# Optimization experiments

Measured on AMD Instinct MI355X. Metric: run time of the kernel, lower is better.

## Reference

```python
import jax, jax.numpy as jnp
import numpy as np

D_MODEL = 1024
NUM_HEADS = 16
BATCH = 2
SEQ = 2048


def setup_inputs() -> dict:
    key = jax.random.key(0)
    ks = jax.random.split(key, 5)
    scale = 1.0 / np.sqrt(D_MODEL)
    x = jax.random.normal(ks[0], (BATCH, SEQ, D_MODEL), dtype=jnp.float32)
    Wq = jax.random.normal(ks[1], (D_MODEL, D_MODEL), dtype=jnp.float32) * scale
    Wk = jax.random.normal(ks[2], (D_MODEL, D_MODEL), dtype=jnp.float32) * scale
    Wv = jax.random.normal(ks[3], (D_MODEL, D_MODEL), dtype=jnp.float32) * scale
    Wo = jax.random.normal(ks[4], (D_MODEL, D_MODEL), dtype=jnp.float32) * scale
    return {"x": x, "Wq": Wq, "Wk": Wk, "Wv": Wv, "Wo": Wo}


def reference(x, Wq, Wk, Wv, Wo):
    b, s, d_model = x.shape
    h = NUM_HEADS
    d_head = d_model // h
    # projections (Linear with weight [out,in]: y = x @ W^T)
    def split_heads(y):
        return y.reshape(b, s, h, d_head).transpose(0, 2, 1, 3)  # b h s d
    q = split_heads(x @ Wq.T)
    k = split_heads(x @ Wk.T)
    v = split_heads(x @ Wv.T)
    # full (non-flash) attention, as in the original
    att = jnp.einsum('bhsd,bhtd->bhst', q, k) / jnp.sqrt(jnp.float32(d_head)).astype(x.dtype)
    att = jax.nn.softmax(att, axis=-1)
    out = jnp.einsum('bhst,bhtd->bhsd', att, v)
    out = out.transpose(0, 2, 1, 3).reshape(b, s, d_model)
    return out @ Wo.T
```

## Files before the change

kernel.cpp:

```cpp
#include <hip/hip_runtime.h>
#include <stdint.h>

typedef __bf16 bf16_t;
typedef __bf16 bf16x4 __attribute__((ext_vector_type(4)));
typedef __bf16 bf16x8 __attribute__((ext_vector_type(8)));
typedef float  f32x4  __attribute__((ext_vector_type(4)));
typedef float  f32x16 __attribute__((ext_vector_type(16)));

#define D_MODEL 1024
#define SEQ     2048
#define BATCH   2
#define NHEAD   16
#define DHEAD   64
#define NROWS   (BATCH*SEQ)
#define LDT     72

#define QSCALE  (0.125f * 1.4426950408889634f)

__device__ __forceinline__ void async_ld16(const bf16_t* g, bf16_t* l) {
    __builtin_amdgcn_global_load_lds(
        (const __attribute__((address_space(1))) uint32_t*)(uintptr_t)g,
        (__attribute__((address_space(3))) uint32_t*)(uintptr_t)l,
        16, 0, 0);
}

__device__ __forceinline__ bf16x8 cvt8(f32x4 lo, f32x4 hi) {
    bf16x8 o;
#pragma unroll
    for (int i = 0; i < 4; ++i) { o[i] = (bf16_t)lo[i]; o[4 + i] = (bf16_t)hi[i]; }
    return o;
}

__device__ __forceinline__ void plswap(uint32_t& a, uint32_t& b) {
    asm("v_permlane32_swap_b32 %0, %1" : "+v"(a), "+v"(b));
}

__global__ void __launch_bounds__(256)
k_cvt(const float* __restrict__ w0, const float* __restrict__ w1,
      const float* __restrict__ w2, const float* __restrict__ w3,
      const float* __restrict__ x,
      bf16_t* __restrict__ o0, bf16_t* __restrict__ o1,
      bf16_t* __restrict__ o2, bf16_t* __restrict__ o3,
      bf16_t* __restrict__ ox)
{
    const int blk = blockIdx.x;
    const float* s; bf16_t* d; int bi;
    if (blk < 2048) { s = x; d = ox; bi = blk; }
    else {
        const int t = blk - 2048, sel = t >> 9; bi = t & 511;
        s = (sel == 0) ? w0 : (sel == 1) ? w1 : (sel == 2) ? w2 : w3;
        d = (sel == 0) ? o0 : (sel == 1) ? o1 : (sel == 2) ? o2 : o3;
    }
    const size_t i = ((size_t)bi * 256 + threadIdx.x) * 8;
    *(bf16x8*)(d + i) = cvt8(*(const f32x4*)(s + i), *(const f32x4*)(s + i + 4));
}

template <int OUT_MODE, int MT, bool DBUF>
__device__ __forceinline__ void gemmT(bf16_t* __restrict__ smem,
                                      const bf16_t* __restrict__ X,
                                      const bf16_t* __restrict__ W,
                                      void* __restrict__ Yv,
                                      int m0, int n0, float oscale)
{
    constexpr int FM  = MT / 32;
    constexpr int BUF = (MT + 128) * 32;

    const int tid  = threadIdx.x;
    const int lane = tid & 63;
    const int w    = tid >> 6;
    const int l15  = lane & 15;
    const int quad = lane >> 4;

    const int cB0 = tid, cB1 = tid + 256;
    const int rB0 = cB0 >> 2, rB1 = cB1 >> 2;
    const int kB0 = (cB0 & 3) ^ ((rB0 >> 1) & 3);
    const int kB1 = (cB1 & 3) ^ ((rB1 >> 1) & 3);
    const bf16_t* gB0 = W + (size_t)(n0 + rB0) * D_MODEL + kB0 * 8;
    const bf16_t* gB1 = W + (size_t)(n0 + rB1) * D_MODEL + kB1 * 8;

    const int cA0 = tid;
    const int rA0 = cA0 >> 2;
    const int kA0 = (cA0 & 3) ^ ((rA0 >> 1) & 3);
    const bf16_t* gA0 = X + (size_t)(m0 + rA0) * D_MODEL + kA0 * 8;
    const int cA1 = tid + 256;
    const int rA1 = cA1 >> 2;
    const int kA1 = (cA1 & 3) ^ ((rA1 >> 1) & 3);
    const bf16_t* gA1 = X + (size_t)(m0 + rA1) * D_MODEL + kA1 * 8;

    int am[FM], bn[4];
    const int mw = (w >> 1) * (MT / 2), nw = (w & 1) * 64;
#pragma unroll
    for (int i = 0; i < FM; ++i) {
        const int ra = mw + i * 16 + l15;
        am[i] = ra * 32 + (quad ^ ((ra >> 1) & 3)) * 8;
    }
#pragma unroll
    for (int i = 0; i < 4; ++i) {
        const int rb = nw + i * 16 + l15;
        bn[i] = rb * 32 + (quad ^ ((rb >> 1) & 3)) * 8;
    }

    f32x4 acc[FM][4];
#pragma unroll
    for (int i = 0; i < FM; ++i)
#pragma unroll
        for (int j = 0; j < 4; ++j) acc[i][j] = f32x4{0.f, 0.f, 0.f, 0.f};

    auto STAGE = [&](int k0, int b) {
        bf16_t* lA = smem + b * BUF;
        bf16_t* lB = lA + MT * 32;
        async_ld16(gA0 + k0, &lA[cA0 * 8]);
        if constexpr (MT == 128) async_ld16(gA1 + k0, &lA[cA1 * 8]);
        async_ld16(gB0 + k0, &lB[cB0 * 8]);
        async_ld16(gB1 + k0, &lB[cB1 * 8]);
    };
    auto COMPUTE = [&](int b) {
        const bf16_t* lA = smem + b * BUF;
        const bf16_t* lB = lA + MT * 32;
        bf16x8 af[FM], bfr[4];
#pragma unroll
        for (int i = 0; i < FM; ++i) af[i] = *(const bf16x8*)&lA[am[i]];
#pragma unroll
        for (int i = 0; i < 4; ++i) bfr[i] = *(const bf16x8*)&lB[bn[i]];
#pragma unroll
        for (int mi = 0; mi < FM; ++mi)
#pragma unroll
            for (int ni = 0; ni < 4; ++ni)
                acc[mi][ni] = __builtin_amdgcn_mfma_f32_16x16x32_bf16(
                    af[mi], bfr[ni], acc[mi][ni], 0, 0, 0);
    };

    if constexpr (DBUF) {
        STAGE(0, 0);
        __syncthreads();
        int buf = 0;
        for (int k0 = 0; k0 < D_MODEL; k0 += 32) {
            if (k0 + 32 < D_MODEL) STAGE(k0 + 32, buf ^ 1);
            COMPUTE(buf);
            __syncthreads();
            buf ^= 1;
        }
    } else {
        for (int k0 = 0; k0 < D_MODEL; k0 += 32) {
            __syncthreads();
            STAGE(k0, 0);
            __syncthreads();
            COMPUTE(0);
        }
    }

    if constexpr (OUT_MODE == 1) {
        bf16_t* lT = smem;
#pragma unroll
        for (int h0 = 0; h0 < 2; ++h0) {
            __syncthreads();
            if ((w >> 1) == h0) {
#pragma unroll
                for (int mi = 0; mi < FM; ++mi)
#pragma unroll
                    for (int ni = 0; ni < 4; ++ni) {
                        bf16x4 pk;
#pragma unroll
                        for (int r = 0; r < 4; ++r)
                            pk[r] = (bf16_t)(acc[mi][ni][r] * oscale);
                        const int col = nw + ni * 16 + l15;
                        *(bf16x4*)&lT[col * LDT + mi * 16 + quad * 4] = pk;
                    }
            }
            __syncthreads();
            const int col = tid & 127;
            const int seg = tid >> 7;
            const int brow = m0 + h0 * 64;
            const int b = brow >> 11, sb = brow & 2047;
            const int cg = n0 + col;
            bf16_t* dst = (bf16_t*)Yv +
                ((size_t)((b << 4) | (cg >> 6)) * 64 + (cg & 63)) * SEQ + sb;
#pragma unroll
            for (int u = 0; u < 4; ++u)
                *(bf16x8*)(dst + seg * 32 + u * 8) =
                    *(const bf16x8*)&lT[col * LDT + seg * 32 + u * 8];
        }
    } else {
#pragma unroll
        for (int mi = 0; mi < FM; ++mi)
#pragma unroll
            for (int ni = 0; ni < 4; ++ni)
#pragma unroll
                for (int r = 0; r < 4; ++r) {
                    const int row = m0 + mw + mi * 16 + quad * 4 + r;
                    const int col = n0 + nw + ni * 16 + l15;
                    const float vv = acc[mi][ni][r] * oscale;
                    if constexpr (OUT_MODE == 0)
                        ((bf16_t*)Yv)[(size_t)row * D_MODEL + col] = (bf16_t)vv;
                    else
                        ((float*)Yv)[(size_t)row * D_MODEL + col] = vv;
                }
    }
}

__global__ void __launch_bounds__(256, 3)
k_gemm_qkv(const bf16_t* __restrict__ X,
           const bf16_t* __restrict__ Wq, const bf16_t* __restrict__ Wk,
           const bf16_t* __restrict__ Wv,
           bf16_t* __restrict__ Qb, bf16_t* __restrict__ Kb, bf16_t* __restrict__ Vt)
{
    __shared__ __align__(16) bf16_t smem[16384];
    const int id = blockIdx.x + 32 * blockIdx.y;
    const int s  = (id & 7) * 96 + (id >> 3);
    const int m0 = (s & 31) * 128;
    const int yp = s >> 5;
    const int sel = yp >> 3;
    const int n0  = (yp & 7) * 128;
    if (sel == 0)      gemmT<0,128,true>(smem, X, Wq, Qb, m0, n0, QSCALE);
    else if (sel == 1) gemmT<0,128,true>(smem, X, Wk, Kb, m0, n0, 1.0f);
    else               gemmT<1,128,true>(smem, X, Wv, Vt, m0, n0, 1.0f);
}

__global__ void __launch_bounds__(256, 2)
k_gemm_out(const bf16_t* __restrict__ X, const bf16_t* __restrict__ W,
           float* __restrict__ Y)
{
    __shared__ __align__(16) bf16_t smem[64 * 32 + 128 * 32];
    const int id = blockIdx.x + 64 * blockIdx.y;
    const int s  = (id & 7) * 64 + (id >> 3);
    const int m0 = (s & 63) * 64;
    const int n0 = (s >> 6) * 128;
    gemmT<2,64,false>(smem, X, W, Y, m0, n0, 1.0f);
}

__global__ void __launch_bounds__(256, 2)
k_attn(const bf16_t* __restrict__ Qb, const bf16_t* __restrict__ Kb,
       const bf16_t* __restrict__ Vt, bf16_t* __restrict__ Ob)
{
    __shared__ __align__(16) char arena[51200];
    bf16_t* lK = (bf16_t*)arena;
    bf16_t* lV = (bf16_t*)(arena + 16384);

    const int tid  = threadIdx.x;
    const int lane = tid & 63;
    const int w    = tid >> 6;
    const int wq   = w >> 1;
    const int wk   = w & 1;
    const int l31  = lane & 31;
    const int h    = lane >> 5;

    const int bh = blockIdx.x;
    const int b_ = bh >> 4, hh = bh & 15;
    const int q0 = blockIdx.y * 128;

    const size_t base = (size_t)b_ * SEQ * D_MODEL + (size_t)hh * DHEAD;
    const bf16_t* Qp = Qb + base;
    const bf16_t* Kp = Kb + base;
    const bf16_t* Vp = Vt + (size_t)bh * DHEAD * SEQ;

    bf16x8 qf[2][4];
#pragma unroll
    for (int qh = 0; qh < 2; ++qh) {
        const int qrow = q0 + wq * 64 + qh * 32 + l31;
#pragma unroll
        for (int c = 0; c < 4; ++c)
            qf[qh][c] = *(const bf16x8*)&Qp[(size_t)qrow * D_MODEL + c * 16 + h * 8];
    }

    const int c0 = tid, c1 = tid + 256;
    const int r0 = c0 >> 3, g0 = (c0 & 7) ^ (r0 & 7);
    const int r1 = r0 + 32;
    const bf16_t* gK0 = Kp + (size_t)r0 * D_MODEL + g0 * 8;
    const bf16_t* gK1 = Kp + (size_t)r1 * D_MODEL + g0 * 8;
    const bf16_t* gV0 = Vp + (size_t)r0 * SEQ + g0 * 8;
    const bf16_t* gV1 = Vp + (size_t)r1 * SEQ + g0 * 8;

    int koff[4], voff[2][2];
#pragma unroll
    for (int c = 0; c < 4; ++c) {
        const int row = wk * 32 + l31;
        koff[c] = row * 64 + (((2 * c + h) ^ (row & 7)) * 8);
    }
#pragma unroll
    for (int a = 0; a < 2; ++a)
#pragma unroll
        for (int ck = 0; ck < 2; ++ck) {
            const int row = a * 32 + l31;
            const int ch  = 4 * wk + 2 * ck + h;
            voff[a][ck] = row * 64 + ((ch ^ (row & 7)) * 8);
        }

    bf16x8 onef;
#pragma unroll
    for (int i = 0; i < 8; ++i) onef[i] = (bf16_t)1.0f;

    f32x16 acc_o[2][2];
    f32x16 acc_s[2];
#pragma unroll
    for (int qh = 0; qh < 2; ++qh) {
#pragma unroll
        for (int i = 0; i < 16; ++i) {
            acc_o[qh][0][i] = 0.f; acc_o[qh][1][i] = 0.f; acc_s[qh][i] = 0.f;
        }
    }

    async_ld16(gK0, &lK[c0 * 8]);
    async_ld16(gK1, &lK[c1 * 8]);
    async_ld16(gV0, &lV[c0 * 8]);
    async_ld16(gV1, &lV[c1 * 8]);
    asm volatile("s_waitcnt vmcnt(0)\n\ts_barrier" ::: "memory");

    int cur = 0;
    const int NT = SEQ / 64;
    for (int t = 0; t < NT; ++t) {
        if (t + 1 < NT) {
            const int kv0 = (t + 1) * 64;
            const int nb = (cur ^ 1) * 4096;
            async_ld16(gK0 + (size_t)kv0 * D_MODEL, &lK[nb + c0 * 8]);
            async_ld16(gK1 + (size_t)kv0 * D_MODEL, &lK[nb + c1 * 8]);
            async_ld16(gV0 + kv0, &lV[nb + c0 * 8]);
            async_ld16(gV1 + kv0, &lV[nb + c1 * 8]);
        }
        const bf16_t* lKc = lK + cur * 4096;
        const bf16_t* lVc = lV + cur * 4096;

        bf16x8 kf[4];
#pragma unroll
        for (int c = 0; c < 4; ++c) kf[c] = *(const bf16x8*)&lKc[koff[c]];

        f32x16 st[2];
#pragma unroll
        for (int qh = 0; qh < 2; ++qh)
#pragma unroll
            for (int i = 0; i < 16; ++i) st[qh][i] = 0.f;
        __builtin_amdgcn_s_setprio(1);
#pragma unroll
        for (int qh = 0; qh < 2; ++qh)
#pragma unroll
            for (int c = 0; c < 4; ++c)
                st[qh] = __builtin_amdgcn_mfma_f32_32x32x16_bf16(
                    kf[c], qf[qh][c], st[qh], 0, 0, 0);
        __builtin_amdgcn_s_setprio(0);

        bf16x4 pk[2][4];
#pragma unroll
        for (int qh = 0; qh < 2; ++qh)
#pragma unroll
            for (int g = 0; g < 4; ++g)
#pragma unroll
                for (int r = 0; r < 4; ++r)
                    pk[qh][g][r] = (bf16_t)__builtin_amdgcn_exp2f(st[qh][g * 4 + r]);

        bf16x8 pf[2][2];
#pragma unroll
        for (int qh = 0; qh < 2; ++qh)
#pragma unroll
            for (int ck = 0; ck < 2; ++ck) {
                union { bf16x4 v; uint32_t d[2]; } ua, ub;
                ua.v = pk[qh][2 * ck];
                ub.v = pk[qh][2 * ck + 1];
                uint32_t a0 = ua.d[0], b0 = ub.d[0];
                uint32_t a1 = ua.d[1], b1 = ub.d[1];
                plswap(a0, b0);
                plswap(a1, b1);
                union { bf16x8 v; uint32_t d[4]; } up;
                up.d[0] = a0; up.d[1] = a1; up.d[2] = b0; up.d[3] = b1;
                pf[qh][ck] = up.v;
            }

        __builtin_amdgcn_s_setprio(1);
#pragma unroll
        for (int qh = 0; qh < 2; ++qh)
#pragma unroll
            for (int ck = 0; ck < 2; ++ck)
                acc_s[qh] = __builtin_amdgcn_mfma_f32_32x32x16_bf16(
                    pf[qh][ck], onef, acc_s[qh], 0, 0, 0);
#pragma unroll
        for (int a = 0; a < 2; ++a)
#pragma unroll
            for (int ck = 0; ck < 2; ++ck) {
                bf16x8 vf = *(const bf16x8*)&lVc[voff[a][ck]];
#pragma unroll
                for (int qh = 0; qh < 2; ++qh)
                    acc_o[qh][a] = __builtin_amdgcn_mfma_f32_32x32x16_bf16(
                        pf[qh][ck], vf, acc_o[qh][a], 0, 0, 0);
            }
        __builtin_amdgcn_s_setprio(0);

        asm volatile("s_waitcnt vmcnt(0) lgkmcnt(0)\n\ts_barrier" ::: "memory");
        cur ^= 1;
    }

    union F16 { f32x16 v; f32x4 q[4]; };
    float* blob = (float*)arena + ((size_t)(wq * 64 + lane)) * 100;

    if (wk) {
#pragma unroll
        for (int qh = 0; qh < 2; ++qh) {
#pragma unroll
            for (int a = 0; a < 2; ++a) {
                F16 u; u.v = acc_o[qh][a];
#pragma unroll
                for (int i = 0; i < 4; ++i)
                    *(f32x4*)&blob[(qh * 8 + a * 4 + i) * 4] = u.q[i];
            }
            F16 s; s.v = acc_s[qh];
#pragma unroll
            for (int i = 0; i < 4; ++i)
                *(f32x4*)&blob[64 + (qh * 4 + i) * 4] = s.q[i];
        }
    }
    __syncthreads();
    if (!wk) {
#pragma unroll
        for (int qh = 0; qh < 2; ++qh) {
#pragma unroll
            for (int a = 0; a < 2; ++a) {
                F16 u; u.v = acc_o[qh][a];
#pragma unroll
                for (int i = 0; i < 4; ++i)
                    u.q[i] += *(const f32x4*)&blob[(qh * 8 + a * 4 + i) * 4];
                acc_o[qh][a] = u.v;
            }
            F16 s; s.v = acc_s[qh];
#pragma unroll
            for (int i = 0; i < 4; ++i)
                s.q[i] += *(const f32x4*)&blob[64 + (qh * 4 + i) * 4];
            acc_s[qh] = s.v;
        }

#pragma unroll
        for (int qh = 0; qh < 2; ++qh)
#pragma unroll
            for (int g = 0; g < 4; ++g)
#pragma unroll
                for (int r = 0; r < 4; ++r) {
                    const float inv = 1.0f / acc_s[qh][g * 4 + r];
                    const int row = b_ * SEQ + q0 + wq * 64 + qh * 32 + (r + 8 * g + 4 * h);
                    const size_t rb = (size_t)row * D_MODEL + hh * DHEAD + l31;
                    Ob[rb]      = (bf16_t)(acc_o[qh][0][g * 4 + r] * inv);
                    Ob[rb + 32] = (bf16_t)(acc_o[qh][1][g * 4 + r] * inv);
                }
    }
}

extern "C" void kernel_launch(void* const* d_in, const int* in_sizes, int n_in,
                              void* d_out, int out_size, void* d_ws, size_t ws_size,
                              hipStream_t stream)
{
    const float* x  = (const float*)d_in[0];
    const float* Wq = (const float*)d_in[1];
    const float* Wk = (const float*)d_in[2];
    const float* Wv = (const float*)d_in[3];
    const float* Wo = (const float*)d_in[4];
    float* out = (float*)d_out;

    const size_t wmat = (size_t)D_MODEL * D_MODEL;
    const size_t mat  = (size_t)NROWS * D_MODEL;
    bf16_t* Wqb = (bf16_t*)d_ws;
    bf16_t* Wkb = Wqb + wmat;
    bf16_t* Wvb = Wkb + wmat;
    bf16_t* Wob = Wvb + wmat;
    bf16_t* Xb  = Wob + wmat;
    bf16_t* Qb  = Xb + mat;
    bf16_t* Kb  = Qb + mat;
    bf16_t* Vt  = Kb + mat;
    bf16_t* Ab  = Qb;

    dim3 blk(256);
    k_cvt<<<dim3(4096), blk, 0, stream>>>(Wq, Wk, Wv, Wo, x, Wqb, Wkb, Wvb, Wob, Xb);
    k_gemm_qkv<<<dim3(32, 24), blk, 0, stream>>>(Xb, Wqb, Wkb, Wvb, Qb, Kb, Vt);
    k_attn<<<dim3(32, 16), blk, 0, stream>>>(Qb, Kb, Vt, Ab);
    k_gemm_out<<<dim3(64, 8), blk, 0, stream>>>(Ab, Wob, out);
}
```

Before: 179.1 us.

## Replace MFMA row-sum with scalar exp accumulation, retile output GEMM, drop swizzles

In the attention kernel, the softmax denominator was computed by an extra MFMA against a ones vector each tile. It is now accumulated in f32 from the exp values and combined with a lane shuffle and a shared-memory exchange, removing two MFMAs per tile and two accumulator register sets. The output GEMM moves from 64x128 to 128x128 tiles with occupancy hint 3, halving the grid. The block-index swizzles for L2 locality are removed from both GEMMs, which may reduce cache reuse.

```diff
diff --git a/kernel.cpp b/kernel.cpp
--- a/kernel.cpp
+++ b/kernel.cpp
@@ -205,27 +205,20 @@
            bf16_t* __restrict__ Qb, bf16_t* __restrict__ Kb, bf16_t* __restrict__ Vt)
 {
     __shared__ __align__(16) bf16_t smem[16384];
-    const int id = blockIdx.x + 32 * blockIdx.y;
-    const int s  = (id & 7) * 96 + (id >> 3);
-    const int m0 = (s & 31) * 128;
-    const int yp = s >> 5;
-    const int sel = yp >> 3;
-    const int n0  = (yp & 7) * 128;
+    const int sel = blockIdx.y >> 3;
+    const int n0  = (blockIdx.y & 7) * 128;
+    const int m0  = blockIdx.x * 128;
     if (sel == 0)      gemmT<0,128,true>(smem, X, Wq, Qb, m0, n0, QSCALE);
     else if (sel == 1) gemmT<0,128,true>(smem, X, Wk, Kb, m0, n0, 1.0f);
     else               gemmT<1,128,true>(smem, X, Wv, Vt, m0, n0, 1.0f);
 }
 
-__global__ void __launch_bounds__(256, 2)
+__global__ void __launch_bounds__(256, 3)
 k_gemm_out(const bf16_t* __restrict__ X, const bf16_t* __restrict__ W,
            float* __restrict__ Y)
 {
-    __shared__ __align__(16) bf16_t smem[64 * 32 + 128 * 32];
-    const int id = blockIdx.x + 64 * blockIdx.y;
-    const int s  = (id & 7) * 64 + (id >> 3);
-    const int m0 = (s & 63) * 64;
-    const int n0 = (s >> 6) * 128;
-    gemmT<2,64,false>(smem, X, W, Y, m0, n0, 1.0f);
+    __shared__ __align__(16) bf16_t smem[(128 + 128) * 32];
+    gemmT<2,128,false>(smem, X, W, Y, blockIdx.x * 128, blockIdx.y * 128, 1.0f);
 }
 
 __global__ void __launch_bounds__(256, 2)
@@ -285,19 +278,12 @@
             voff[a][ck] = row * 64 + ((ch ^ (row & 7)) * 8);
         }
 
-    bf16x8 onef;
-#pragma unroll
-    for (int i = 0; i < 8; ++i) onef[i] = (bf16_t)1.0f;
-
     f32x16 acc_o[2][2];
-    f32x16 acc_s[2];
-#pragma unroll
-    for (int qh = 0; qh < 2; ++qh) {
-#pragma unroll
-        for (int i = 0; i < 16; ++i) {
-            acc_o[qh][0][i] = 0.f; acc_o[qh][1][i] = 0.f; acc_s[qh][i] = 0.f;
-        }
-    }
+    float rsumf[2] = {0.f, 0.f};
+#pragma unroll
+    for (int qh = 0; qh < 2; ++qh)
+#pragma unroll
+        for (int i = 0; i < 16; ++i) { acc_o[qh][0][i] = 0.f; acc_o[qh][1][i] = 0.f; }
 
     async_ld16(gK0, &lK[c0 * 8]);
     async_ld16(gK1, &lK[c1 * 8]);
@@ -341,10 +327,15 @@
 #pragma unroll
         for (int qh = 0; qh < 2; ++qh)
 #pragma unroll
-            for (int g = 0; g < 4; ++g)
-#pragma unroll
-                for (int r = 0; r < 4; ++r)
-                    pk[qh][g][r] = (bf16_t)__builtin_amdgcn_exp2f(st[qh][g * 4 + r]);
+            for (int g = 0; g < 4; ++g) {
+                const float e0 = __builtin_amdgcn_exp2f(st[qh][g * 4 + 0]);
+                const float e1 = __builtin_amdgcn_exp2f(st[qh][g * 4 + 1]);
+                const float e2 = __builtin_amdgcn_exp2f(st[qh][g * 4 + 2]);
+                const float e3 = __builtin_amdgcn_exp2f(st[qh][g * 4 + 3]);
+                pk[qh][g][0] = (bf16_t)e0; pk[qh][g][1] = (bf16_t)e1;
+                pk[qh][g][2] = (bf16_t)e2; pk[qh][g][3] = (bf16_t)e3;
+                rsumf[qh] += (e0 + e1) + (e2 + e3);
+            }
 
         bf16x8 pf[2][2];
 #pragma unroll
@@ -365,12 +356,6 @@
 
         __builtin_amdgcn_s_setprio(1);
 #pragma unroll
-        for (int qh = 0; qh < 2; ++qh)
-#pragma unroll
-            for (int ck = 0; ck < 2; ++ck)
-                acc_s[qh] = __builtin_amdgcn_mfma_f32_32x32x16_bf16(
-                    pf[qh][ck], onef, acc_s[qh], 0, 0, 0);
-#pragma unroll
         for (int a = 0; a < 2; ++a)
 #pragma unroll
             for (int ck = 0; ck < 2; ++ck) {
@@ -386,12 +371,17 @@
         cur ^= 1;
     }
 
+#pragma unroll
+    for (int qh = 0; qh < 2; ++qh)
+        rsumf[qh] += __shfl_xor(rsumf[qh], 32);
+
     union F16 { f32x16 v; f32x4 q[4]; };
-    float* blob = (float*)arena + ((size_t)(wq * 64 + lane)) * 100;
+    float* blob = (float*)arena + ((size_t)(wq * 64 + lane)) * 68;
+    float* sbuf = (float*)(arena + 34816);
 
     if (wk) {
 #pragma unroll
-        for (int qh = 0; qh < 2; ++qh) {
+        for (int qh = 0; qh < 2; ++qh)
 #pragma unroll
             for (int a = 0; a < 2; ++a) {
                 F16 u; u.v = acc_o[qh][a];
@@ -399,16 +389,13 @@
                 for (int i = 0; i < 4; ++i)
                     *(f32x4*)&blob[(qh * 8 + a * 4 + i) * 4] = u.q[i];
             }
-            F16 s; s.v = acc_s[qh];
-#pragma unroll
-            for (int i = 0; i < 4; ++i)
-                *(f32x4*)&blob[64 + (qh * 4 + i) * 4] = s.q[i];
-        }
+        blob[64] = rsumf[0];
+        blob[65] = rsumf[1];
     }
     __syncthreads();
     if (!wk) {
 #pragma unroll
-        for (int qh = 0; qh < 2; ++qh) {
+        for (int qh = 0; qh < 2; ++qh)
 #pragma unroll
             for (int a = 0; a < 2; ++a) {
                 F16 u; u.v = acc_o[qh][a];
@@ -417,21 +404,24 @@
                     u.q[i] += *(const f32x4*)&blob[(qh * 8 + a * 4 + i) * 4];
                 acc_o[qh][a] = u.v;
             }
-            F16 s; s.v = acc_s[qh];
-#pragma unroll
-            for (int i = 0; i < 4; ++i)
-                s.q[i] += *(const f32x4*)&blob[64 + (qh * 4 + i) * 4];
-            acc_s[qh] = s.v;
-        }
-
+        rsumf[0] += blob[64];
+        rsumf[1] += blob[65];
+        if (h == 0) {
+            sbuf[wq * 64 + l31]      = rsumf[0];
+            sbuf[wq * 64 + 32 + l31] = rsumf[1];
+        }
+    }
+    __syncthreads();
+    if (!wk) {
 #pragma unroll
         for (int qh = 0; qh < 2; ++qh)
 #pragma unroll
             for (int g = 0; g < 4; ++g)
 #pragma unroll
                 for (int r = 0; r < 4; ++r) {
-                    const float inv = 1.0f / acc_s[qh][g * 4 + r];
-                    const int row = b_ * SEQ + q0 + wq * 64 + qh * 32 + (r + 8 * g + 4 * h);
+                    const int rl = r + 8 * g + 4 * h;
+                    const float inv = 1.0f / sbuf[wq * 64 + qh * 32 + rl];
+                    const int row = b_ * SEQ + q0 + wq * 64 + qh * 32 + rl;
                     const size_t rb = (size_t)row * D_MODEL + hh * DHEAD + l31;
                     Ob[rb]      = (bf16_t)(acc_o[qh][0][g * 4 + r] * inv);
                     Ob[rb + 32] = (bf16_t)(acc_o[qh][1][g * 4 + r] * inv);
@@ -466,5 +456,5 @@
     k_cvt<<<dim3(4096), blk, 0, stream>>>(Wq, Wk, Wv, Wo, x, Wqb, Wkb, Wvb, Wob, Xb);
     k_gemm_qkv<<<dim3(32, 24), blk, 0, stream>>>(Xb, Wqb, Wkb, Wvb, Qb, Kb, Vt);
     k_attn<<<dim3(32, 16), blk, 0, stream>>>(Qb, Kb, Vt, Ab);
-    k_gemm_out<<<dim3(64, 8), blk, 0, stream>>>(Ab, Wob, out);
-}
+    k_gemm_out<<<dim3(32, 8), blk, 0, stream>>>(Ab, Wob, out);
+}
```

Measured after the change: 178.2 us. About the same (-0.5%).
